# Performance work log

Measured on AMD Instinct MI355X. Metric: run time of the kernel, lower is better.

## Reference

```python
import jax, jax.numpy as jnp
import numpy as np

N, DF, DR, H, K = 4096, 128, 64, 1024, 10


def _init_linear(key, fan_in, fan_out):
    kw, kb = jax.random.split(key)
    bound = 1.0 / np.sqrt(fan_in)
    W = jax.random.uniform(kw, (fan_in, fan_out), jnp.float32, -bound, bound)
    b = jax.random.uniform(kb, (fan_out,), jnp.float32, -bound, bound)
    return W, b


def setup_inputs() -> dict:
    key = jax.random.key(0)
    ks = jax.random.split(key, 8)
    condition = jax.random.normal(ks[0], (N, DF), jnp.float32)
    tensor = jax.random.normal(ks[1], (N, DR), jnp.float32)
    Win, b_in = _init_linear(ks[2], DF + DR, H)
    W1, b1 = _init_linear(ks[3], H, H)
    W2, b2 = _init_linear(ks[4], H, H)
    W3, b3 = _init_linear(ks[5], H, H)
    Wout, b_out = _init_linear(ks[6], H, DR)
    return {"condition": condition, "tensor": tensor,
            "Win": Win, "b_in": b_in, "W1": W1, "b1": b1,
            "W2": W2, "b2": b2, "W3": W3, "b3": b3,
            "Wout": Wout, "b_out": b_out}


def _mlp(x, Win, b_in, W1, b1, W2, b2, W3, b3, Wout, b_out):
    # FFNN: input layer + 3 hidden layers with Softplus, linear output -> DR
    h = jax.nn.softplus(x @ Win + b_in)
    h = jax.nn.softplus(h @ W1 + b1)
    h = jax.nn.softplus(h @ W2 + b2)
    h = jax.nn.softplus(h @ W3 + b3)
    return h @ Wout + b_out


def reference(condition, tensor, Win, b_in, W1, b1, W2, b2, W3, b3, Wout, b_out):
    # torch.cdist(condition, condition), p=2 -> [N, N]
    sq = jnp.sum(condition * condition, axis=-1)
    d2 = sq[:, None] + sq[None, :] - 2.0 * (condition @ condition.T)
    dist = jnp.sqrt(jnp.maximum(d2, 0.0))
    # torch.topk(dist, 10, dim=1, largest=False) -> k nearest neighbor indices
    _, neighbor_idx = jax.lax.top_k(-dist, K)  # [N, K]
    # gather neighbor groups
    cond_g = condition[neighbor_idx]  # [N, K, DF]
    tens_g = tensor[neighbor_idx]     # [N, K, DR]
    # MongeMapNetwork.pushforward: tensor - MLP(concat(condition, tensor))
    x = jnp.concatenate([cond_g, tens_g], axis=-1)  # [N, K, DF+DR]
    pushed = tens_g - _mlp(x, Win, b_in, W1, b1, W2, b2, W3, b3, Wout, b_out)
    return pushed  # [N, K, DR]
```

## Files before the change

### kernel.cpp

```cpp
#include <hip/hip_runtime.h>
#include <stdint.h>

typedef unsigned short u16;
typedef unsigned int   u32;
typedef unsigned long long u64;
typedef short v8bf __attribute__((ext_vector_type(8)));
typedef float v4f  __attribute__((ext_vector_type(4)));

#define NPTS 4096
#define DF   128
#define DR   64
#define HID  1024
#define KNN  10
#define DIN  192

#define AS1 __attribute__((address_space(1)))
#define AS3 __attribute__((address_space(3)))

__device__ __forceinline__ float bf2f(u16 b){ return __uint_as_float(((unsigned)b)<<16); }
__device__ __forceinline__ u16 f2bf(float f){
  unsigned u = __float_as_uint(f);
  unsigned r = 0x7fffu + ((u>>16)&1u);
  return (u16)((u + r)>>16);
}
__device__ __forceinline__ float softplus_f(float x){
  return x>15.f ? x : __logf(1.f + __expf(x));
}
__device__ __forceinline__ float rdv(const void* p, long j, int fl){
  return fl ? bf2f(((const u16*)p)[j]) : ((const float*)p)[j];
}
__device__ __forceinline__ void gl2lds16(const u16* g, u16* l){
  __builtin_amdgcn_global_load_lds((const AS1 unsigned int*)g, (AS3 unsigned int*)l, 16, 0, 0);
}

__global__ void detect_k(const u16* __restrict__ c, int* __restrict__ flag){
  __shared__ int cnt[256];
  int t = threadIdx.x, n = 0;
  for(int i=t; i<8192; i+=256){
    u16 v = c[2*i];
    int e = (v>>7)&0xff;
    n += (e>=96 && e<=158);
  }
  cnt[t] = n; __syncthreads();
  for(int s=128; s>0; s>>=1){ if(t<s) cnt[t]+=cnt[t+s]; __syncthreads(); }
  if(t==0) *flag = (cnt[0] > 4915) ? 1 : 0;
}

__global__ void prep_k(const void* cond, const void* tens,
    const void* Wi, const void* W1, const void* W2, const void* W3, const void* Wo,
    const void* bi, const void* b1, const void* b2, const void* b3, const void* bo,
    float* __restrict__ condF, float* __restrict__ tensF, float* __restrict__ biasF,
    u16* Oi, u16* O1, u16* O2, u16* O3, u16* Oo,
    float* __restrict__ sq, u16* __restrict__ X, const int* __restrict__ flag){
  __shared__ u16 tile[32][33];
  const int fl = *flag;
  const int bid = blockIdx.x, tid = threadIdx.x;
  if(bid < 3089){
    int i = bid*256 + tid;
    if(i < 524288){ condF[i] = rdv(cond, i, fl); }
    else if(i < 786432){ tensF[i-524288] = rdv(tens, i-524288, fl); }
    else{
      int j = i - 786432;
      if(j < 1024)      biasF[j] = rdv(bi, j, fl);
      else if(j < 2048) biasF[j] = rdv(b1, j-1024, fl);
      else if(j < 3072) biasF[j] = rdv(b2, j-2048, fl);
      else if(j < 4096) biasF[j] = rdv(b3, j-3072, fl);
      else if(j < 4160) biasF[j] = rdv(bo, j-4096, fl);
    }
  } else if(bid < 6417){
    int b = bid - 3089;
    const void* in; u16* out; int R, C, bx, by;
    if(b < 192)      {              in=Wi; out=Oi; R=192;  C=1024; bx=b&31; by=b>>5; }
    else if(b < 1216){ b -= 192;    in=W1; out=O1; R=1024; C=1024; bx=b&31; by=b>>5; }
    else if(b < 2240){ b -= 1216;   in=W2; out=O2; R=1024; C=1024; bx=b&31; by=b>>5; }
    else if(b < 3264){ b -= 2240;   in=W3; out=O3; R=1024; C=1024; bx=b&31; by=b>>5; }
    else             { b -= 3264;   in=Wo; out=Oo; R=1024; C=64;   bx=b&1;  by=b>>1; }
    int gx = bx*32, gy = by*32;
    int tx = tid&31, ty = tid>>5;
    #pragma unroll
    for(int r=ty; r<32; r+=8){
      size_t idx = (size_t)(gy+r)*C + gx + tx;
      tile[r][tx] = fl ? ((const u16*)in)[idx] : f2bf(((const float*)in)[idx]);
    }
    __syncthreads();
    #pragma unroll
    for(int r=ty; r<32; r+=8) out[(size_t)(gx+r)*R + gy + tx] = tile[tx][r];
  } else if(bid < 7441){
    int b = bid - 6417;
    int row = b*4 + (tid>>6), lane = tid&63;
    float a = rdv(cond, (long)row*DF + lane, fl);
    float c2 = rdv(cond, (long)row*DF + lane + 64, fl);
    double s = (double)a*a + (double)c2*c2;
    #pragma unroll
    for(int off=32; off>0; off>>=1) s += __shfl_down(s, off, 64);
    if(lane==0) sq[row] = (float)s;
  } else {
    int c = (bid-7441)*256 + tid;
    int j = c/48;
    int off = (c - j*48)*4;
    ushort4 o;
    if(off < DF){
      o.x = f2bf(rdv(cond, (long)j*DF + off + 0, fl));
      o.y = f2bf(rdv(cond, (long)j*DF + off + 1, fl));
      o.z = f2bf(rdv(cond, (long)j*DF + off + 2, fl));
      o.w = f2bf(rdv(cond, (long)j*DF + off + 3, fl));
    }else{
      int t2 = off - DF;
      o.x = f2bf(rdv(tens, (long)j*DR + t2 + 0, fl));
      o.y = f2bf(rdv(tens, (long)j*DR + t2 + 1, fl));
      o.z = f2bf(rdv(tens, (long)j*DR + t2 + 2, fl));
      o.w = f2bf(rdv(tens, (long)j*DR + t2 + 3, fl));
    }
    *(ushort4*)&X[(size_t)j*DIN + off] = o;
  }
}

__device__ __forceinline__ void gemm_bt_body(const u16* __restrict__ A,
    const u16* __restrict__ Bt, const float* __restrict__ bias, u16* __restrict__ C,
    int Nc, int Kc, int bid, u16* As, u16* Bs){
  const int xcd = bid&7, slot = bid>>3;
  const int bm = (xcd*4 + (slot>>4)) * 128;
  const int bn = (slot&15) * 64;
  const int tid = threadIdx.x, lane = tid&63, wave = tid>>6;
  const int wm = (wave&1)*64, wn = (wave>>1)*32;
  int c0 = wave*128 + lane, c1 = c0 + 64;
  int r0 = c0>>2, q0 = c0&3, r1 = c1>>2, q1 = c1&3;
  int cb = wave*64 + lane, rb = cb>>2, qb = cb&3;
  const u16* pA0 = A  + (size_t)(bm+r0)*Kc + q0*8;
  const u16* pA1 = A  + (size_t)(bm+r1)*Kc + q1*8;
  const u16* pB  = Bt + (size_t)(bn+rb)*Kc + qb*8;
  u16* lA0 = &As[(wave*128      )*8];
  u16* lA1 = &As[(wave*128 + 64 )*8];
  u16* lB  = &Bs[(wave*64       )*8];
  const int m16 = lane&15, q = lane>>4;
  v4f acc[4][2] = {};
  for(int kb=0; kb<Kc; kb+=32){
    gl2lds16(pA0 + kb, lA0);
    gl2lds16(pA1 + kb, lA1);
    gl2lds16(pB  + kb, lB);
    __syncthreads();
    v8bf a[4], b[2];
    #pragma unroll
    for(int x=0;x<4;x++) a[x] = *(const v8bf*)&As[(wm + x*16 + m16)*32 + q*8];
    #pragma unroll
    for(int x=0;x<2;x++) b[x] = *(const v8bf*)&Bs[(wn + x*16 + m16)*32 + q*8];
    #pragma unroll
    for(int mi=0;mi<4;mi++)
      #pragma unroll
      for(int ni=0;ni<2;ni++)
        acc[mi][ni] = __builtin_amdgcn_mfma_f32_16x16x32_bf16(a[mi], b[ni], acc[mi][ni], 0,0,0);
    __syncthreads();
  }
  const int col16 = lane&15, rowq = lane>>4;
  #pragma unroll
  for(int mi=0;mi<4;mi++){
    #pragma unroll
    for(int ni=0;ni<2;ni++){
      int cn = bn + wn + ni*16 + col16;
      float bi = bias[cn];
      #pragma unroll
      for(int r=0;r<4;r++){
        int rw = bm + wm + mi*16 + rowq*4 + r;
        float v = softplus_f(acc[mi][ni][r] + bi);
        C[(size_t)rw*Nc + cn] = f2bf(v);
      }
    }
  }
}

__device__ __forceinline__ void knn_body(const float* __restrict__ dist,
    const float* __restrict__ condF, int* __restrict__ nidx, int row,
    float* __restrict__ af, int* __restrict__ scnt,
    int* __restrict__ cand, u64* __restrict__ keys){
  const int lane = threadIdx.x&63;
  af[lane]    = condF[(size_t)row*DF + lane];
  af[lane+64] = condF[(size_t)row*DF + lane + 64];
  if(lane==0) *scnt = 0;
  const float4* drow4 = (const float4*)(dist + (size_t)row*NPTS);
  float4 vals[16];
  #pragma unroll
  for(int k=0;k<16;k++) vals[k] = drow4[lane + k*64];
  float mx = 0.f;
  #pragma unroll
  for(int k=0;k<16;k++)
    mx = fmaxf(mx, fmaxf(fmaxf(vals[k].x,vals[k].y), fmaxf(vals[k].z,vals[k].w)));
  #pragma unroll
  for(int off=32; off>0; off>>=1) mx = fmaxf(mx, __shfl_down(mx, off, 64));
  mx = __shfl(mx, 0, 64);
  float hi = mx*1.000001f + 1e-6f, lo = 0.f;
  for(int it=0; it<18; ++it){
    float mid = 0.5f*(lo+hi);
    int c = 0;
    #pragma unroll
    for(int k=0;k<16;k++)
      c += (vals[k].x<mid) + (vals[k].y<mid) + (vals[k].z<mid) + (vals[k].w<mid);
    #pragma unroll
    for(int off=32; off>0; off>>=1) c += __shfl_down(c, off, 64);
    c = __shfl(c, 0, 64);
    if(c >= 16){ hi = mid; if(c <= 48) break; }
    else lo = mid;
  }
  const float t = hi;
  #pragma unroll
  for(int k=0;k<16;k++){
    float v[4] = {vals[k].x, vals[k].y, vals[k].z, vals[k].w};
    #pragma unroll
    for(int e=0;e<4;e++){
      if(v[e] < t){
        int s = atomicAdd(scnt, 1);
        if(s < 64) cand[s] = (lane + k*64)*4 + e;
      }
    }
  }
  int cnt = *scnt; if(cnt > 64) cnt = 64;
  u64 mykey = ~0ULL; int myj = -1;
  if(lane < cnt){
    int j = cand[lane];
    const float4* bp4 = (const float4*)(condF + (size_t)j*DF);
    double s = 0.0;
    #pragma unroll
    for(int v4i=0; v4i<32; v4i++){
      float4 bv = bp4[v4i];
      double d0 = (double)af[v4i*4+0]-(double)bv.x;
      double d1 = (double)af[v4i*4+1]-(double)bv.y;
      double d2 = (double)af[v4i*4+2]-(double)bv.z;
      double d3 = (double)af[v4i*4+3]-(double)bv.w;
      s += d0*d0 + d1*d1 + d2*d2 + d3*d3;
    }
    u64 bits = (u64)__double_as_longlong(s);
    mykey = (bits & ~0xFFFULL) | (u32)j;
    myj = j;
  }
  keys[lane] = mykey;
  if(lane < cnt){
    int rank = 0;
    for(int c2=0;c2<cnt;c2++) rank += (keys[c2] < mykey);
    if(rank < KNN) nidx[row*KNN + rank] = myj;
  }
}

__global__ __launch_bounds__(256,2) void gram_g1_k(const u16* __restrict__ condB,
    const float* __restrict__ condF, const float* __restrict__ sq,
    float* __restrict__ dist, const int* __restrict__ flag,
    const u16* __restrict__ X, const u16* __restrict__ Wt_in,
    const float* __restrict__ biasF, u16* __restrict__ A0){
  __shared__ __align__(16) u16 smem[20480];
  const int bid = blockIdx.x;
  if(bid < 512){
    gemm_bt_body(X, Wt_in, biasF, A0, HID, DIN, bid, smem, smem+4096);
    return;
  }
  const int gb = bid - 512;
  u16* Ahi = smem;
  u16* Alo = smem + 5120;
  u16* Bhi = smem + 10240;
  u16* Blo = smem + 15360;
  const int fl = *flag;
  const int bm = (gb&31)*128, bn = (gb>>5)*128;
  const int tid = threadIdx.x, lane = tid&63, wave = tid>>6;
  const int wm = (wave&1)*64, wn = (wave>>1)*64;
  v4f acc[4][4] = {};
  for(int kb=0; kb<DF; kb+=32){
    if(fl){
      #pragma unroll
      for(int t=0;t<2;t++){
        int c2 = tid + t*256;
        int r = c2>>2, col = (c2&3)*8;
        *(uint4*)&Ahi[r*40+col] = *(const uint4*)&condB[(size_t)(bm+r)*DF + kb + col];
        *(uint4*)&Bhi[r*40+col] = *(const uint4*)&condB[(size_t)(bn+r)*DF + kb + col];
      }
    }else{
      #pragma unroll
      for(int t=0;t<4;t++){
        int ch = tid + t*256;
        int r = ch>>3, c = (ch&7)*4;
        float4 av = *(const float4*)&condF[(size_t)(bm+r)*DF + kb + c];
        float4 bv = *(const float4*)&condF[(size_t)(bn+r)*DF + kb + c];
        ushort4 ah, bh, al, bl;
        ah.x=f2bf(av.x); ah.y=f2bf(av.y); ah.z=f2bf(av.z); ah.w=f2bf(av.w);
        bh.x=f2bf(bv.x); bh.y=f2bf(bv.y); bh.z=f2bf(bv.z); bh.w=f2bf(bv.w);
        al.x=f2bf(av.x-bf2f(ah.x)); al.y=f2bf(av.y-bf2f(ah.y));
        al.z=f2bf(av.z-bf2f(ah.z)); al.w=f2bf(av.w-bf2f(ah.w));
        bl.x=f2bf(bv.x-bf2f(bh.x)); bl.y=f2bf(bv.y-bf2f(bh.y));
        bl.z=f2bf(bv.z-bf2f(bh.z)); bl.w=f2bf(bv.w-bf2f(bh.w));
        *(ushort4*)&Ahi[r*40+c] = ah; *(ushort4*)&Bhi[r*40+c] = bh;
        *(ushort4*)&Alo[r*40+c] = al; *(ushort4*)&Blo[r*40+c] = bl;
      }
    }
    __syncthreads();
    const int m16 = lane&15, q = lane>>4;
    v8bf ahf[4], bhf[4];
    #pragma unroll
    for(int x=0;x<4;x++){
      ahf[x] = *(const v8bf*)&Ahi[(wm + x*16 + m16)*40 + q*8];
      bhf[x] = *(const v8bf*)&Bhi[(wn + x*16 + m16)*40 + q*8];
    }
    if(!fl){
      v8bf alf[4], blf[4];
      #pragma unroll
      for(int x=0;x<4;x++){
        alf[x] = *(const v8bf*)&Alo[(wm + x*16 + m16)*40 + q*8];
        blf[x] = *(const v8bf*)&Blo[(wn + x*16 + m16)*40 + q*8];
      }
      #pragma unroll
      for(int mi=0;mi<4;mi++)
        #pragma unroll
        for(int ni=0;ni<4;ni++){
          acc[mi][ni] = __builtin_amdgcn_mfma_f32_16x16x32_bf16(alf[mi], bhf[ni], acc[mi][ni], 0,0,0);
          acc[mi][ni] = __builtin_amdgcn_mfma_f32_16x16x32_bf16(ahf[mi], blf[ni], acc[mi][ni], 0,0,0);
        }
    }
    #pragma unroll
    for(int mi=0;mi<4;mi++)
      #pragma unroll
      for(int ni=0;ni<4;ni++)
        acc[mi][ni] = __builtin_amdgcn_mfma_f32_16x16x32_bf16(ahf[mi], bhf[ni], acc[mi][ni], 0,0,0);
    __syncthreads();
  }
  const int col16 = lane&15, rowq = lane>>4;
  #pragma unroll
  for(int mi=0;mi<4;mi++){
    #pragma unroll
    for(int ni=0;ni<4;ni++){
      int cj = bn + wn + ni*16 + col16;
      float sqj = sq[cj];
      #pragma unroll
      for(int r=0;r<4;r++){
        int ri = bm + wm + mi*16 + rowq*4 + r;
        float d2 = (sq[ri] + sqj) - 2.0f*acc[mi][ni][r];
        dist[(size_t)ri*NPTS + cj] = fmaxf(d2, 0.f);
      }
    }
  }
}

__global__ __launch_bounds__(256,2) void gemm_knn_k(const u16* __restrict__ A,
    const u16* __restrict__ Bt, const float* __restrict__ bias, u16* __restrict__ C,
    const float* __restrict__ dist, const float* __restrict__ condF,
    int* __restrict__ nidx, int rowoff){
  __shared__ __align__(16) u16 gsm[6144];
  __shared__ float af[4][DF];
  __shared__ int   scnt[4];
  __shared__ int   cand[4][64];
  __shared__ u64   keys[4][64];
  const int bid = blockIdx.x;
  if(bid < 512){
    gemm_bt_body(A, Bt, bias, C, HID, HID, bid, gsm, gsm+4096);
  } else {
    const int wv = threadIdx.x>>6;
    const int row = rowoff + (bid-512)*4 + wv;
    knn_body(dist, condF, nidx, row, af[wv], &scnt[wv], cand[wv], keys[wv]);
  }
}

__global__ __launch_bounds__(256,2) void gemm_bt_k(const u16* __restrict__ A,
    const u16* __restrict__ Bt, const float* __restrict__ bias, u16* __restrict__ C){
  __shared__ __align__(16) u16 As[128*32];
  __shared__ __align__(16) u16 Bs[64*32];
  gemm_bt_body(A, Bt, bias, C, HID, HID, blockIdx.x, As, Bs);
}

__global__ __launch_bounds__(256,2) void gemm_out_k(const u16* __restrict__ A,
    const u16* __restrict__ Bt, float* __restrict__ Pp){
  __shared__ __align__(16) u16 As[128*32];
  __shared__ __align__(16) u16 Bs[64*32];
  const int bm = (blockIdx.x>>2)*128;
  const int k0 = (blockIdx.x&3)*256;
  float* P = Pp + (size_t)(blockIdx.x&3)*262144;
  const int tid = threadIdx.x, lane = tid&63, wave = tid>>6;
  const int wm = wave*32;
  int c0 = wave*128 + lane, c1 = c0 + 64;
  int ra0 = c0>>2, qa0 = c0&3, ra1 = c1>>2, qa1 = c1&3;
  int cb = wave*64 + lane;
  int rb = cb>>2, qb = cb&3;
  const u16* pA0 = A  + (size_t)(bm+ra0)*HID + qa0*8;
  const u16* pA1 = A  + (size_t)(bm+ra1)*HID + qa1*8;
  const u16* pB  = Bt + (size_t)rb*HID + qb*8;
  u16* lA0 = &As[(wave*128     )*8];
  u16* lA1 = &As[(wave*128 + 64)*8];
  u16* lB  = &Bs[(wave*64      )*8];
  const int m16 = lane&15, q = lane>>4;
  v4f acc[2][4] = {};
  for(int kb=k0; kb<k0+256; kb+=32){
    gl2lds16(pA0 + kb, lA0);
    gl2lds16(pA1 + kb, lA1);
    gl2lds16(pB  + kb, lB);
    __syncthreads();
    v8bf a[2], b[4];
    a[0] = *(const v8bf*)&As[(wm + m16)*32 + q*8];
    a[1] = *(const v8bf*)&As[(wm + 16 + m16)*32 + q*8];
    #pragma unroll
    for(int x=0;x<4;x++) b[x] = *(const v8bf*)&Bs[(x*16 + m16)*32 + q*8];
    #pragma unroll
    for(int mi=0;mi<2;mi++)
      #pragma unroll
      for(int ni=0;ni<4;ni++)
        acc[mi][ni] = __builtin_amdgcn_mfma_f32_16x16x32_bf16(a[mi], b[ni], acc[mi][ni], 0,0,0);
    __syncthreads();
  }
  const int col16 = lane&15, rowq = lane>>4;
  #pragma unroll
  for(int mi=0;mi<2;mi++){
    #pragma unroll
    for(int ni=0;ni<4;ni++){
      int cn = ni*16 + col16;
      #pragma unroll
      for(int r=0;r<4;r++){
        int rw = bm + wm + mi*16 + rowq*4 + r;
        P[(size_t)rw*DR + cn] = acc[mi][ni][r];
      }
    }
  }
}

__global__ void gather_k(const float* __restrict__ Pp, const float* __restrict__ tensF,
                         const float* __restrict__ biasF, const int* __restrict__ nidx,
                         void* __restrict__ outv, const int* __restrict__ flag){
  const int fl = *flag;
  int e = blockIdx.x*256 + threadIdx.x;
  int m = e>>4;
  int c = (e&15)*4;
  int j = nidx[m] & (NPTS-1);
  size_t rc = (size_t)j*DR + c;
  float4 t  = *(const float4*)&tensF[rc];
  float4 b  = *(const float4*)&biasF[4096 + c];
  float4 p0 = *(const float4*)&Pp[rc];
  float4 p1 = *(const float4*)&Pp[262144 + rc];
  float4 p2 = *(const float4*)&Pp[524288 + rc];
  float4 p3 = *(const float4*)&Pp[786432 + rc];
  float4 v;
  v.x = t.x - (b.x + ((p0.x+p1.x)+(p2.x+p3.x)));
  v.y = t.y - (b.y + ((p0.y+p1.y)+(p2.y+p3.y)));
  v.z = t.z - (b.z + ((p0.z+p1.z)+(p2.z+p3.z)));
  v.w = t.w - (b.w + ((p0.w+p1.w)+(p2.w+p3.w)));
  if(fl){
    ushort4 o; o.x=f2bf(v.x); o.y=f2bf(v.y); o.z=f2bf(v.z); o.w=f2bf(v.w);
    *(ushort4*)&((u16*)outv)[(size_t)m*DR + c] = o;
  }else{
    *(float4*)&((float*)outv)[(size_t)m*DR + c] = v;
  }
}

constexpr size_t OFF_FLAG  = 0;
constexpr size_t OFF_SQ    = 256;
constexpr size_t OFF_NIDX  = OFF_SQ    + 16384;
constexpr size_t OFF_BIAS  = OFF_NIDX  + 163840;
constexpr size_t OFF_CONDF = OFF_BIAS  + 16640;
constexpr size_t OFF_TENSF = OFF_CONDF + 2097152;
constexpr size_t OFF_WTIN  = OFF_TENSF + 1048576;
constexpr size_t OFF_WT1   = OFF_WTIN  + 393216;
constexpr size_t OFF_WT2   = OFF_WT1   + 2097152;
constexpr size_t OFF_WT3   = OFF_WT2   + 2097152;
constexpr size_t OFF_WTO   = OFF_WT3   + 2097152;
constexpr size_t OFF_DIST  = OFF_WTO   + 131072;
constexpr size_t OFF_X     = OFF_DIST  + 67108864;
constexpr size_t OFF_A0    = OFF_X     + 1572864;
constexpr size_t OFF_A1    = OFF_A0    + 8388608;
constexpr size_t OFF_P     = OFF_A1    + 8388608;

extern "C" void kernel_launch(void* const* d_in, const int* in_sizes, int n_in,
                              void* d_out, int out_size, void* d_ws, size_t ws_size,
                              hipStream_t stream){
  char* ws = (char*)d_ws;
  int*   flag  = (int*)  (ws + OFF_FLAG);
  float* sqv   = (float*)(ws + OFF_SQ);
  int*   nidx  = (int*)  (ws + OFF_NIDX);
  float* biasF = (float*)(ws + OFF_BIAS);
  float* condF = (float*)(ws + OFF_CONDF);
  float* tensF = (float*)(ws + OFF_TENSF);
  u16*   Wt_in = (u16*)  (ws + OFF_WTIN);
  u16*   Wt1   = (u16*)  (ws + OFF_WT1);
  u16*   Wt2   = (u16*)  (ws + OFF_WT2);
  u16*   Wt3   = (u16*)  (ws + OFF_WT3);
  u16*   Wt_o  = (u16*)  (ws + OFF_WTO);
  float* dist  = (float*)(ws + OFF_DIST);
  u16*   X     = (u16*)  (ws + OFF_X);
  u16*   A0    = (u16*)  (ws + OFF_A0);
  u16*   A1    = (u16*)  (ws + OFF_A1);
  float* Pp    = (float*)(ws + OFF_P);

  detect_k <<<1, 256, 0, stream>>>((const u16*)d_in[0], flag);
  prep_k   <<<8209, 256, 0, stream>>>(d_in[0], d_in[1],
                d_in[2], d_in[4], d_in[6], d_in[8], d_in[10],
                d_in[3], d_in[5], d_in[7], d_in[9], d_in[11],
                condF, tensF, biasF, Wt_in, Wt1, Wt2, Wt3, Wt_o, sqv, X, flag);
  gram_g1_k<<<1536, 256, 0, stream>>>((const u16*)d_in[0], condF, sqv, dist, flag,
                                      X, Wt_in, biasF, A0);
  gemm_knn_k<<<1024, 256, 0, stream>>>(A0, Wt1, biasF+1024, A1, dist, condF, nidx, 0);
  gemm_knn_k<<<1024, 256, 0, stream>>>(A1, Wt2, biasF+2048, A0, dist, condF, nidx, 2048);
  gemm_bt_k  <<<512, 256, 0, stream>>>(A0, Wt3, biasF+3072, A1);
  gemm_out_k <<<128, 256, 0, stream>>>(A1, Wt_o, Pp);
  gather_k   <<<2560, 256, 0, stream>>>(Pp, tensF, biasF, nidx, d_out, flag);
}
```

Measured before the change: 214.6 us.

## Store distance matrix as fp16 and enlarge hidden GEMM tiles to 128x128

The squared-distance matrix is now written as fp16 instead of fp32, which halves its write and read traffic. The kNN candidate search does its threshold bisection on the raw fp16 bit patterns as unsigned integers, and the final ranking still uses exact double-precision distances. Separately, the hidden-layer GEMM tile grows from 128x64 to 128x128 per workgroup, with a new block-to-tile mapping. This halves the number of GEMM blocks and increases reuse per LDS load, at the cost of more accumulator registers and fewer GEMM blocks to overlap with the kNN blocks. fp16 may lose ordering resolution near the threshold, but a window of 16 to 48 candidates is kept, so the top-10 should stay correct.

```diff
diff --git a/kernel.cpp b/kernel.cpp
--- a/kernel.cpp
+++ b/kernel.cpp
@@ -1,4 +1,5 @@
 #include <hip/hip_runtime.h>
+#include <hip/hip_fp16.h>
 #include <stdint.h>
 
 typedef unsigned short u16;
@@ -6,6 +7,7 @@
 typedef unsigned long long u64;
 typedef short v8bf __attribute__((ext_vector_type(8)));
 typedef float v4f  __attribute__((ext_vector_type(4)));
+typedef u16   v8u  __attribute__((ext_vector_type(8)));
 
 #define NPTS 4096
 #define DF   128
@@ -22,6 +24,10 @@
   unsigned u = __float_as_uint(f);
   unsigned r = 0x7fffu + ((u>>16)&1u);
   return (u16)((u + r)>>16);
+}
+__device__ __forceinline__ u16 f2h(float f){
+  __half h = __float2half(f);
+  return __half_as_ushort(h);
 }
 __device__ __forceinline__ float softplus_f(float x){
   return x>15.f ? x : __logf(1.f + __expf(x));
@@ -115,39 +121,40 @@
   }
 }
 
-__device__ __forceinline__ void gemm_bt_body(const u16* __restrict__ A,
+__device__ __forceinline__ void gemm128_body(const u16* __restrict__ A,
     const u16* __restrict__ Bt, const float* __restrict__ bias, u16* __restrict__ C,
-    int Nc, int Kc, int bid, u16* As, u16* Bs){
-  const int xcd = bid&7, slot = bid>>3;
-  const int bm = (xcd*4 + (slot>>4)) * 128;
-  const int bn = (slot&15) * 64;
-  const int tid = threadIdx.x, lane = tid&63, wave = tid>>6;
-  const int wm = (wave&1)*64, wn = (wave>>1)*32;
-  int c0 = wave*128 + lane, c1 = c0 + 64;
-  int r0 = c0>>2, q0 = c0&3, r1 = c1>>2, q1 = c1&3;
-  int cb = wave*64 + lane, rb = cb>>2, qb = cb&3;
-  const u16* pA0 = A  + (size_t)(bm+r0)*Kc + q0*8;
-  const u16* pA1 = A  + (size_t)(bm+r1)*Kc + q1*8;
-  const u16* pB  = Bt + (size_t)(bn+rb)*Kc + qb*8;
-  u16* lA0 = &As[(wave*128      )*8];
-  u16* lA1 = &As[(wave*128 + 64 )*8];
-  u16* lB  = &Bs[(wave*64       )*8];
+    int Kc, int bid, u16* As, u16* Bs){
+  const int wg = (bid&7)*32 + (bid>>3);
+  const int bm = (wg>>3)*128, bn = (wg&7)*128;
+  const int lane = threadIdx.x&63, wave = threadIdx.x>>6;
+  const int wm = (wave&1)*64, wn = (wave>>1)*64;
+  const int sr = wave*32 + (lane>>2), sc = (lane&3)*8;
+  const u16* pA0 = A  + (size_t)(bm+sr   )*Kc + sc;
+  const u16* pA1 = A  + (size_t)(bm+sr+16)*Kc + sc;
+  const u16* pB0 = Bt + (size_t)(bn+sr   )*Kc + sc;
+  const u16* pB1 = Bt + (size_t)(bn+sr+16)*Kc + sc;
+  u16* lA0 = &As[wave*1024];
+  u16* lA1 = &As[wave*1024 + 512];
+  u16* lB0 = &Bs[wave*1024];
+  u16* lB1 = &Bs[wave*1024 + 512];
   const int m16 = lane&15, q = lane>>4;
-  v4f acc[4][2] = {};
+  v4f acc[4][4] = {};
   for(int kb=0; kb<Kc; kb+=32){
     gl2lds16(pA0 + kb, lA0);
     gl2lds16(pA1 + kb, lA1);
-    gl2lds16(pB  + kb, lB);
-    __syncthreads();
-    v8bf a[4], b[2];
-    #pragma unroll
-    for(int x=0;x<4;x++) a[x] = *(const v8bf*)&As[(wm + x*16 + m16)*32 + q*8];
-    #pragma unroll
-    for(int x=0;x<2;x++) b[x] = *(const v8bf*)&Bs[(wn + x*16 + m16)*32 + q*8];
+    gl2lds16(pB0 + kb, lB0);
+    gl2lds16(pB1 + kb, lB1);
+    __syncthreads();
+    v8bf a[4], b[4];
+    #pragma unroll
+    for(int x=0;x<4;x++){
+      a[x] = *(const v8bf*)&As[(wm + x*16 + m16)*32 + q*8];
+      b[x] = *(const v8bf*)&Bs[(wn + x*16 + m16)*32 + q*8];
+    }
     #pragma unroll
     for(int mi=0;mi<4;mi++)
       #pragma unroll
-      for(int ni=0;ni<2;ni++)
+      for(int ni=0;ni<4;ni++)
         acc[mi][ni] = __builtin_amdgcn_mfma_f32_16x16x32_bf16(a[mi], b[ni], acc[mi][ni], 0,0,0);
     __syncthreads();
   }
@@ -155,20 +162,20 @@
   #pragma unroll
   for(int mi=0;mi<4;mi++){
     #pragma unroll
-    for(int ni=0;ni<2;ni++){
+    for(int ni=0;ni<4;ni++){
       int cn = bn + wn + ni*16 + col16;
       float bi = bias[cn];
       #pragma unroll
       for(int r=0;r<4;r++){
         int rw = bm + wm + mi*16 + rowq*4 + r;
         float v = softplus_f(acc[mi][ni][r] + bi);
-        C[(size_t)rw*Nc + cn] = f2bf(v);
-      }
-    }
-  }
-}
-
-__device__ __forceinline__ void knn_body(const float* __restrict__ dist,
+        C[(size_t)rw*HID + cn] = f2bf(v);
+      }
+    }
+  }
+}
+
+__device__ __forceinline__ void knn_body(const u16* __restrict__ distH,
     const float* __restrict__ condF, int* __restrict__ nidx, int row,
     float* __restrict__ af, int* __restrict__ scnt,
     int* __restrict__ cand, u64* __restrict__ keys){
@@ -176,42 +183,44 @@
   af[lane]    = condF[(size_t)row*DF + lane];
   af[lane+64] = condF[(size_t)row*DF + lane + 64];
   if(lane==0) *scnt = 0;
-  const float4* drow4 = (const float4*)(dist + (size_t)row*NPTS);
-  float4 vals[16];
-  #pragma unroll
-  for(int k=0;k<16;k++) vals[k] = drow4[lane + k*64];
-  float mx = 0.f;
-  #pragma unroll
-  for(int k=0;k<16;k++)
-    mx = fmaxf(mx, fmaxf(fmaxf(vals[k].x,vals[k].y), fmaxf(vals[k].z,vals[k].w)));
-  #pragma unroll
-  for(int off=32; off>0; off>>=1) mx = fmaxf(mx, __shfl_down(mx, off, 64));
-  mx = __shfl(mx, 0, 64);
-  float hi = mx*1.000001f + 1e-6f, lo = 0.f;
-  for(int it=0; it<18; ++it){
-    float mid = 0.5f*(lo+hi);
+  const v8u* drow = (const v8u*)(distH + (size_t)row*NPTS);
+  v8u vals[8];
+  #pragma unroll
+  for(int k=0;k<8;k++) vals[k] = drow[lane + k*64];
+  u32 mx = 0;
+  #pragma unroll
+  for(int k=0;k<8;k++)
+    #pragma unroll
+    for(int e=0;e<8;e++){ u32 v = vals[k][e]; mx = v>mx ? v : mx; }
+  #pragma unroll
+  for(int off=32; off>0; off>>=1){
+    u32 o = (u32)__shfl_down((int)mx, off, 64); mx = o>mx ? o : mx;
+  }
+  mx = (u32)__shfl((int)mx, 0, 64);
+  u32 hi = mx+1, lo = 0;
+  for(int it=0; it<17; ++it){
+    u32 mid = (lo+hi)>>1;
     int c = 0;
     #pragma unroll
-    for(int k=0;k<16;k++)
-      c += (vals[k].x<mid) + (vals[k].y<mid) + (vals[k].z<mid) + (vals[k].w<mid);
+    for(int k=0;k<8;k++)
+      #pragma unroll
+      for(int e=0;e<8;e++) c += ((u32)vals[k][e] < mid);
     #pragma unroll
     for(int off=32; off>0; off>>=1) c += __shfl_down(c, off, 64);
     c = __shfl(c, 0, 64);
     if(c >= 16){ hi = mid; if(c <= 48) break; }
     else lo = mid;
   }
-  const float t = hi;
-  #pragma unroll
-  for(int k=0;k<16;k++){
-    float v[4] = {vals[k].x, vals[k].y, vals[k].z, vals[k].w};
-    #pragma unroll
-    for(int e=0;e<4;e++){
-      if(v[e] < t){
+  const u32 t = hi;
+  #pragma unroll
+  for(int k=0;k<8;k++)
+    #pragma unroll
+    for(int e=0;e<8;e++){
+      if((u32)vals[k][e] < t){
         int s = atomicAdd(scnt, 1);
-        if(s < 64) cand[s] = (lane + k*64)*4 + e;
-      }
-    }
-  }
+        if(s < 64) cand[s] = (lane + k*64)*8 + e;
+      }
+    }
   int cnt = *scnt; if(cnt > 64) cnt = 64;
   u64 mykey = ~0ULL; int myj = -1;
   if(lane < cnt){
@@ -241,16 +250,16 @@
 
 __global__ __launch_bounds__(256,2) void gram_g1_k(const u16* __restrict__ condB,
     const float* __restrict__ condF, const float* __restrict__ sq,
-    float* __restrict__ dist, const int* __restrict__ flag,
+    u16* __restrict__ distH, const int* __restrict__ flag,
     const u16* __restrict__ X, const u16* __restrict__ Wt_in,
     const float* __restrict__ biasF, u16* __restrict__ A0){
   __shared__ __align__(16) u16 smem[20480];
   const int bid = blockIdx.x;
-  if(bid < 512){
-    gemm_bt_body(X, Wt_in, biasF, A0, HID, DIN, bid, smem, smem+4096);
+  if(bid < 256){
+    gemm128_body(X, Wt_in, biasF, A0, DIN, bid, smem, smem+4096);
     return;
   }
-  const int gb = bid - 512;
+  const int gb = bid - 256;
   u16* Ahi = smem;
   u16* Alo = smem + 5120;
   u16* Bhi = smem + 10240;
@@ -328,7 +337,7 @@
       for(int r=0;r<4;r++){
         int ri = bm + wm + mi*16 + rowq*4 + r;
         float d2 = (sq[ri] + sqj) - 2.0f*acc[mi][ni][r];
-        dist[(size_t)ri*NPTS + cj] = fmaxf(d2, 0.f);
+        distH[(size_t)ri*NPTS + cj] = f2h(fmaxf(d2, 0.f));
       }
     }
   }
@@ -336,28 +345,28 @@
 
 __global__ __launch_bounds__(256,2) void gemm_knn_k(const u16* __restrict__ A,
     const u16* __restrict__ Bt, const float* __restrict__ bias, u16* __restrict__ C,
-    const float* __restrict__ dist, const float* __restrict__ condF,
+    const u16* __restrict__ distH, const float* __restrict__ condF,
     int* __restrict__ nidx, int rowoff){
-  __shared__ __align__(16) u16 gsm[6144];
+  __shared__ __align__(16) u16 gsm[8192];
   __shared__ float af[4][DF];
   __shared__ int   scnt[4];
   __shared__ int   cand[4][64];
   __shared__ u64   keys[4][64];
   const int bid = blockIdx.x;
-  if(bid < 512){
-    gemm_bt_body(A, Bt, bias, C, HID, HID, bid, gsm, gsm+4096);
+  if(bid < 256){
+    gemm128_body(A, Bt, bias, C, HID, bid, gsm, gsm+4096);
   } else {
     const int wv = threadIdx.x>>6;
-    const int row = rowoff + (bid-512)*4 + wv;
-    knn_body(dist, condF, nidx, row, af[wv], &scnt[wv], cand[wv], keys[wv]);
+    const int row = rowoff + (bid-256)*4 + wv;
+    knn_body(distH, condF, nidx, row, af[wv], &scnt[wv], cand[wv], keys[wv]);
   }
 }
 
 __global__ __launch_bounds__(256,2) void gemm_bt_k(const u16* __restrict__ A,
     const u16* __restrict__ Bt, const float* __restrict__ bias, u16* __restrict__ C){
-  __shared__ __align__(16) u16 As[128*32];
-  __shared__ __align__(16) u16 Bs[64*32];
-  gemm_bt_body(A, Bt, bias, C, HID, HID, blockIdx.x, As, Bs);
+  __shared__ __align__(16) u16 As[4096];
+  __shared__ __align__(16) u16 Bs[4096];
+  gemm128_body(A, Bt, bias, C, HID, blockIdx.x, As, Bs);
 }
 
 __global__ __launch_bounds__(256,2) void gemm_out_k(const u16* __restrict__ A,
@@ -453,7 +462,7 @@
 constexpr size_t OFF_WT3   = OFF_WT2   + 2097152;
 constexpr size_t OFF_WTO   = OFF_WT3   + 2097152;
 constexpr size_t OFF_DIST  = OFF_WTO   + 131072;
-constexpr size_t OFF_X     = OFF_DIST  + 67108864;
+constexpr size_t OFF_X     = OFF_DIST  + 33554432;
 constexpr size_t OFF_A0    = OFF_X     + 1572864;
 constexpr size_t OFF_A1    = OFF_A0    + 8388608;
 constexpr size_t OFF_P     = OFF_A1    + 8388608;
@@ -473,7 +482,7 @@
   u16*   Wt2   = (u16*)  (ws + OFF_WT2);
   u16*   Wt3   = (u16*)  (ws + OFF_WT3);
   u16*   Wt_o  = (u16*)  (ws + OFF_WTO);
-  float* dist  = (float*)(ws + OFF_DIST);
+  u16*   distH = (u16*)  (ws + OFF_DIST);
   u16*   X     = (u16*)  (ws + OFF_X);
   u16*   A0    = (u16*)  (ws + OFF_A0);
   u16*   A1    = (u16*)  (ws + OFF_A1);
@@ -484,11 +493,11 @@
                 d_in[2], d_in[4], d_in[6], d_in[8], d_in[10],
                 d_in[3], d_in[5], d_in[7], d_in[9], d_in[11],
                 condF, tensF, biasF, Wt_in, Wt1, Wt2, Wt3, Wt_o, sqv, X, flag);
-  gram_g1_k<<<1536, 256, 0, stream>>>((const u16*)d_in[0], condF, sqv, dist, flag,
+  gram_g1_k<<<1280, 256, 0, stream>>>((const u16*)d_in[0], condF, sqv, distH, flag,
                                       X, Wt_in, biasF, A0);
-  gemm_knn_k<<<1024, 256, 0, stream>>>(A0, Wt1, biasF+1024, A1, dist, condF, nidx, 0);
-  gemm_knn_k<<<1024, 256, 0, stream>>>(A1, Wt2, biasF+2048, A0, dist, condF, nidx, 2048);
-  gemm_bt_k  <<<512, 256, 0, stream>>>(A0, Wt3, biasF+3072, A1);
+  gemm_knn_k<<<768, 256, 0, stream>>>(A0, Wt1, biasF+1024, A1, distH, condF, nidx, 0);
+  gemm_knn_k<<<768, 256, 0, stream>>>(A1, Wt2, biasF+2048, A0, distH, condF, nidx, 2048);
+  gemm_bt_k  <<<256, 256, 0, stream>>>(A0, Wt3, biasF+3072, A1);
   gemm_out_k <<<128, 256, 0, stream>>>(A1, Wt_o, Pp);
   gather_k   <<<2560, 256, 0, stream>>>(Pp, tensF, biasF, nidx, d_out, flag);
 }
```

Result: slower. 221.5 us (+3.2%).
